# Optimization experiments

Hardware: AMD Instinct MI355X
Metric: run time of the kernel (lower is better)

The kernel has to match this reference:

```python
import jax, jax.numpy as jnp
import numpy as np

B, D, Q, K, C = 1024, 512, 131072, 32, 10
TEMP = 0.1
EPS = 1e-12  # F.normalize eps


def setup_inputs() -> dict:
    key = jax.random.key(0)
    k1, k2, k3 = jax.random.split(key, 3)
    x = jax.random.normal(k1, (B, D), dtype=jnp.float32)
    memory = jax.random.normal(k2, (Q, D), dtype=jnp.float32)
    # queue entries are stored L2-normalized (see update_queue)
    memory = memory / jnp.linalg.norm(memory, axis=1, keepdims=True)
    memory_label = jax.random.randint(k3, (Q,), 0, C, dtype=jnp.int32)
    return {"x": x, "memory": memory, "memory_label": memory_label}


def reference(x, memory, memory_label):
    # cosine similarity: normalize queries, bank already normalized
    xn = x / jnp.maximum(jnp.linalg.norm(x, axis=1, keepdims=True), EPS)
    dist = xn @ memory.T                      # [B, Q]
    sim_weight, sim_indices = jax.lax.top_k(dist, K)   # [B, K]
    sim_labels = memory_label[sim_indices]              # [B, K] gather
    w = jax.nn.softmax(sim_weight / TEMP, axis=1)       # [B, K]
    one_hot = jax.nn.one_hot(sim_labels, C, dtype=w.dtype)  # [B, K, C]
    pred_scores = jnp.einsum('bkc,bk->bc', one_hot, w)       # softmax vote
    return jnp.minimum(pred_scores + 1e-5, 1.0)
```

## Files before the change

### kernel.cpp

```cpp
#include <hip/hip_runtime.h>

typedef unsigned short u16;
typedef unsigned char u8;
typedef __attribute__((ext_vector_type(4))) float f32x4;

#define B_ROWS 1024
#define DIM 512
#define QN 131072
#define TOPK 32
#define NCLS 10
#define TAUS 35.84f
#define CAP 1024
#define FP8SCALE 16.0f

#define S_VMCNT(N) asm volatile("s_waitcnt vmcnt(" #N ")" ::: "memory")
#define S_BAR() asm volatile("s_barrier" ::: "memory")
#define S_LGKM0() asm volatile("s_waitcnt lgkmcnt(0)" ::: "memory")

__device__ __forceinline__ void gload_lds16(const void* gsrc, void* ldst) {
  __builtin_amdgcn_global_load_lds(
      (const __attribute__((address_space(1))) void*)gsrc,
      (__attribute__((address_space(3))) void*)ldst, 16, 0, 0);
}

__device__ __forceinline__ int pk4(float a, float b, float c, float d) {
  int w = __builtin_amdgcn_cvt_pk_fp8_f32(a, b, 0, false);
  w = __builtin_amdgcn_cvt_pk_fp8_f32(c, d, w, true);
  return w;
}

__global__ __launch_bounds__(256) void normalize_x(const float* __restrict__ x,
                                                   float* __restrict__ xn,
                                                   u8* __restrict__ xnb8,
                                                   int* __restrict__ cnt) {
  int row = blockIdx.x;
  int tid = threadIdx.x;
  __shared__ float xs[DIM];
  __shared__ float wsum[4];
  if (tid == 0) cnt[row] = 0;
  float2 v = ((const float2*)(x + (size_t)row * DIM))[tid];
  float ss = v.x * v.x + v.y * v.y;
  #pragma unroll
  for (int o = 32; o; o >>= 1) ss += __shfl_xor(ss, o);
  if ((tid & 63) == 0) wsum[tid >> 6] = ss;
  __syncthreads();
  float tot = wsum[0] + wsum[1] + wsum[2] + wsum[3];
  float scale = 1.0f / fmaxf(sqrtf(tot), 1e-12f);
  float2 o2; o2.x = v.x * scale; o2.y = v.y * scale;
  ((float2*)(xn + (size_t)row * DIM))[tid] = o2;
  xs[2 * tid] = o2.x; xs[2 * tid + 1] = o2.y;
  __syncthreads();
  if (tid < 32) {
    int c = tid >> 2, t4 = tid & 3;
    int k0 = c * 64 + t4 * 8;
    int4 w;
    w.x = pk4(xs[k0+0]*FP8SCALE, xs[k0+1]*FP8SCALE, xs[k0+2]*FP8SCALE, xs[k0+3]*FP8SCALE);
    w.y = pk4(xs[k0+4]*FP8SCALE, xs[k0+5]*FP8SCALE, xs[k0+6]*FP8SCALE, xs[k0+7]*FP8SCALE);
    w.z = pk4(xs[k0+32]*FP8SCALE, xs[k0+33]*FP8SCALE, xs[k0+34]*FP8SCALE, xs[k0+35]*FP8SCALE);
    w.w = pk4(xs[k0+36]*FP8SCALE, xs[k0+37]*FP8SCALE, xs[k0+38]*FP8SCALE, xs[k0+39]*FP8SCALE);
    ((int4*)(xnb8 + (size_t)row * DIM))[tid] = w;
  }
}

__global__ __launch_bounds__(256, 3) void gemm_filter(const u8* __restrict__ xnb8,
                                                      const float* __restrict__ mem,
                                                      int* __restrict__ cnt,
                                                      int* __restrict__ ccol) {
  __shared__ __attribute__((aligned(16))) u8 As[2][16384];
  __shared__ __attribute__((aligned(16))) u8 Bs[2][4096];
  int bid = blockIdx.x;
  int xcd = bid & 7;
  int i = bid >> 3;
  int colt = xcd * 256 + (i >> 2);
  int rowt = i & 3;
  int row0 = rowt * 256;
  int col0 = colt * 64;
  int tid = threadIdx.x;
  int lane = tid & 63;
  int wv = tid >> 6;

  int sg = (tid & 3) ^ ((tid >> 3) & 3);
  const u8* gA[4];
  #pragma unroll
  for (int jj = 0; jj < 4; ++jj) {
    int r = jj * 64 + (tid >> 2);
    gA[jj] = xnb8 + (size_t)(row0 + r) * DIM + sg * 16;
  }
  const float* gB = mem + (size_t)(col0 + (tid >> 2)) * DIM + sg * 8;

  int L = lane & 15;
  int g = lane >> 4;
  int phys = g ^ ((L >> 1) & 3);
  int offA = (wv * 64 + L) * 64 + phys * 16;
  int offB = L * 64 + phys * 16;

  f32x4 acc[4][4];
  #pragma unroll
  for (int m = 0; m < 4; ++m)
    #pragma unroll
    for (int n = 0; n < 4; ++n) acc[m][n] = (f32x4){0.f, 0.f, 0.f, 0.f};

  float4 pb[4];

  auto stageA = [&](int h) {
    int slot = h & 1;
    #pragma unroll
    for (int jj = 0; jj < 4; ++jj)
      gload_lds16(gA[jj] + h * 64, &As[slot][jj * 4096 + tid * 16]);
  };
  auto issuePB = [&](int h) {
    const float4* s = (const float4*)(gB + h * 64);
    pb[0] = s[0]; pb[1] = s[1];
    pb[2] = s[8]; pb[3] = s[9];
  };
  auto writeB = [&](int h) {
    int slot = h & 1;
    int4 w;
    w.x = pk4(pb[0].x*FP8SCALE, pb[0].y*FP8SCALE, pb[0].z*FP8SCALE, pb[0].w*FP8SCALE);
    w.y = pk4(pb[1].x*FP8SCALE, pb[1].y*FP8SCALE, pb[1].z*FP8SCALE, pb[1].w*FP8SCALE);
    w.z = pk4(pb[2].x*FP8SCALE, pb[2].y*FP8SCALE, pb[2].z*FP8SCALE, pb[2].w*FP8SCALE);
    w.w = pk4(pb[3].x*FP8SCALE, pb[3].y*FP8SCALE, pb[3].z*FP8SCALE, pb[3].w*FP8SCALE);
    *(int4*)&Bs[slot][tid * 16] = w;
  };

  union I4L { int4 v; long l[2]; };

  stageA(0); issuePB(0);
  S_VMCNT(0);
  writeB(0);
  issuePB(1);
  S_LGKM0();

  #pragma unroll
  for (int h = 0; h < 8; ++h) {
    if (h < 7) { S_VMCNT(4); }
    else { S_VMCNT(0); }
    S_BAR();
    if (h < 7) stageA(h + 1);
    const u8* Ab = &As[h & 1][0];
    const u8* Bb = &Bs[h & 1][0];
    I4L av[4], bv[4];
    #pragma unroll
    for (int m = 0; m < 4; ++m) av[m].v = *(const int4*)(Ab + offA + m * 1024);
    #pragma unroll
    for (int n = 0; n < 4; ++n) bv[n].v = *(const int4*)(Bb + offB + n * 1024);
    __builtin_amdgcn_s_setprio(1);
    #pragma unroll
    for (int m = 0; m < 4; ++m)
      #pragma unroll
      for (int n = 0; n < 4; ++n)
        acc[m][n] = __builtin_amdgcn_mfma_f32_16x16x32_fp8_fp8(
            av[m].l[0], bv[n].l[0], acc[m][n], 0, 0, 0);
    #pragma unroll
    for (int m = 0; m < 4; ++m)
      #pragma unroll
      for (int n = 0; n < 4; ++n)
        acc[m][n] = __builtin_amdgcn_mfma_f32_16x16x32_fp8_fp8(
            av[m].l[1], bv[n].l[1], acc[m][n], 0, 0, 0);
    __builtin_amdgcn_s_setprio(0);
    if (h < 7) {
      S_VMCNT(4);
      writeB(h + 1);
      if (h < 6) issuePB(h + 2);
      S_LGKM0();
    }
  }

  int rbase = row0 + wv * 64 + (lane >> 4) * 4;
  int cbase = col0 + (lane & 15);
  #pragma unroll
  for (int m = 0; m < 4; ++m)
    #pragma unroll
    for (int n = 0; n < 4; ++n)
      #pragma unroll
      for (int q = 0; q < 4; ++q) {
        float v = acc[m][n][q];
        if (v > TAUS) {
          int grow = rbase + m * 16 + q;
          int gcol = cbase + n * 16;
          int idx = atomicAdd(&cnt[grow], 1);
          if (idx < CAP) ccol[(size_t)grow * CAP + idx] = gcol;
        }
      }
}

__global__ __launch_bounds__(256) void rescore_vote(const float* __restrict__ xn,
                                                    const float* __restrict__ mem,
                                                    const int* __restrict__ labels,
                                                    const int* __restrict__ cnt,
                                                    const int* __restrict__ ccol,
                                                    float* __restrict__ out) {
  int row = blockIdx.x;
  int tid = threadIdx.x;
  int gid = tid >> 4;
  int gl = tid & 15;
  __shared__ __attribute__((aligned(16))) float xs[DIM];
  __shared__ double sv[CAP];
  __shared__ int sc[CAP];
  __shared__ double selv[TOPK];
  __shared__ int selc[TOPK];
  __shared__ double wv32[TOPK];
  __shared__ int slab[TOPK];

  ((float2*)xs)[tid] = ((const float2*)(xn + (size_t)row * DIM))[tid];
  if (tid < TOPK) { selv[tid] = -1e300; selc[tid] = 0; }
  int count = cnt[row];
  if (count > CAP) count = CAP;
  __syncthreads();

  for (int c = gid; c < count; c += 16) {
    int col = ccol[(size_t)row * CAP + c];
    const float4* mp = (const float4*)(mem + (size_t)col * DIM);
    const float4* xp = (const float4*)xs;
    double p = 0.0;
    #pragma unroll
    for (int u = 0; u < 8; ++u) {
      float4 mv = mp[u * 16 + gl];
      float4 xv = xp[u * 16 + gl];
      p += (double)mv.x * xv.x + (double)mv.y * xv.y +
           (double)mv.z * xv.z + (double)mv.w * xv.w;
    }
    #pragma unroll
    for (int o = 8; o; o >>= 1) p += __shfl_xor(p, o);
    if (gl == 0) { sv[c] = p; sc[c] = col; }
  }
  __syncthreads();

  for (int c = tid; c < count; c += 256) {
    double v = sv[c]; int cc = sc[c];
    int r = 0;
    for (int j = 0; j < count; ++j) {
      double vj = sv[j]; int cj = sc[j];
      r += (vj > v) || (vj == v && cj < cc);
    }
    if (r < TOPK) { selv[r] = v; selc[r] = cc; }
  }
  __syncthreads();

  if (tid < TOPK) {
    slab[tid] = labels[selc[tid]];
    double e = exp((selv[tid] - selv[0]) * 10.0);
    double s = e;
    #pragma unroll
    for (int o = 16; o; o >>= 1) s += __shfl_xor(s, o, 32);
    wv32[tid] = e / s;
  }
  __syncthreads();
  if (tid < NCLS) {
    double a = 0.0;
    #pragma unroll
    for (int k = 0; k < TOPK; ++k)
      if (slab[k] == tid) a += wv32[k];
    float r2 = (float)(a + 1e-5);
    out[(size_t)row * NCLS + tid] = fminf(r2, 1.0f);
  }
}

extern "C" void kernel_launch(void* const* d_in, const int* in_sizes, int n_in,
                              void* d_out, int out_size, void* d_ws, size_t ws_size,
                              hipStream_t stream) {
  const float* x = (const float*)d_in[0];
  const float* mem = (const float*)d_in[1];
  const int* labels = (const int*)d_in[2];
  float* out = (float*)d_out;
  char* ws = (char*)d_ws;

  float* xn = (float*)ws;
  u8* xnb8 = (u8*)(ws + 2097152);
  int* cnt = (int*)(ws + 2621440);
  int* ccol = (int*)(ws + 2625536);

  normalize_x<<<dim3(B_ROWS), dim3(256), 0, stream>>>(x, xn, xnb8, cnt);
  gemm_filter<<<dim3((B_ROWS / 256) * (QN / 64)), dim3(256), 0, stream>>>(
      xnb8, mem, cnt, ccol);
  rescore_vote<<<dim3(B_ROWS), dim3(256), 0, stream>>>(xn, mem, labels, cnt,
                                                       ccol, out);
}
```

Baseline: 195.8 us.

## Load A fragments directly from global; stage full B tile in LDS once

The A operand (fp8 normalized queries) is now read straight from global memory into registers with a two-slot software prefetch, replacing the LDS staging path. The full 64x512 B tile is converted to fp8 and written to LDS in one prologue, followed by a single barrier, which removes the per-step barriers and waitcnt choreography. Each wave now issues its own global loads for A, with no sharing through LDS, and the B conversion can no longer overlap the MFMA loop. LDS use drops from 40KB to 32KB per block.

```diff
diff --git a/kernel.cpp b/kernel.cpp
--- a/kernel.cpp
+++ b/kernel.cpp
@@ -12,16 +12,6 @@
 #define TAUS 35.84f
 #define CAP 1024
 #define FP8SCALE 16.0f
-
-#define S_VMCNT(N) asm volatile("s_waitcnt vmcnt(" #N ")" ::: "memory")
-#define S_BAR() asm volatile("s_barrier" ::: "memory")
-#define S_LGKM0() asm volatile("s_waitcnt lgkmcnt(0)" ::: "memory")
-
-__device__ __forceinline__ void gload_lds16(const void* gsrc, void* ldst) {
-  __builtin_amdgcn_global_load_lds(
-      (const __attribute__((address_space(1))) void*)gsrc,
-      (__attribute__((address_space(3))) void*)ldst, 16, 0, 0);
-}
 
 __device__ __forceinline__ int pk4(float a, float b, float c, float d) {
   int w = __builtin_amdgcn_cvt_pk_fp8_f32(a, b, 0, false);
@@ -66,8 +56,7 @@
                                                       const float* __restrict__ mem,
                                                       int* __restrict__ cnt,
                                                       int* __restrict__ ccol) {
-  __shared__ __attribute__((aligned(16))) u8 As[2][16384];
-  __shared__ __attribute__((aligned(16))) u8 Bs[2][4096];
+  __shared__ __attribute__((aligned(16))) u8 Bs[8][4096];
   int bid = blockIdx.x;
   int xcd = bid & 7;
   int i = bid >> 3;
@@ -79,20 +68,34 @@
   int lane = tid & 63;
   int wv = tid >> 6;
 
-  int sg = (tid & 3) ^ ((tid >> 3) & 3);
-  const u8* gA[4];
-  #pragma unroll
-  for (int jj = 0; jj < 4; ++jj) {
-    int r = jj * 64 + (tid >> 2);
-    gA[jj] = xnb8 + (size_t)(row0 + r) * DIM + sg * 16;
-  }
-  const float* gB = mem + (size_t)(col0 + (tid >> 2)) * DIM + sg * 8;
+  {
+    int r = tid >> 2, s = tid & 3;
+    int phys = s ^ ((r >> 1) & 3);
+    const float* src = mem + (size_t)(col0 + r) * DIM + s * 8;
+    u8* dst = &Bs[0][r * 64 + phys * 16];
+    #pragma unroll
+    for (int h = 0; h < 8; ++h) {
+      const float4* sp = (const float4*)(src + h * 64);
+      float4 f0 = sp[0], f1 = sp[1];
+      const float4* sp2 = (const float4*)(src + h * 64 + 32);
+      float4 f2 = sp2[0], f3 = sp2[1];
+      int4 w;
+      w.x = pk4(f0.x*FP8SCALE, f0.y*FP8SCALE, f0.z*FP8SCALE, f0.w*FP8SCALE);
+      w.y = pk4(f1.x*FP8SCALE, f1.y*FP8SCALE, f1.z*FP8SCALE, f1.w*FP8SCALE);
+      w.z = pk4(f2.x*FP8SCALE, f2.y*FP8SCALE, f2.z*FP8SCALE, f2.w*FP8SCALE);
+      w.w = pk4(f3.x*FP8SCALE, f3.y*FP8SCALE, f3.z*FP8SCALE, f3.w*FP8SCALE);
+      *(int4*)(dst + h * 4096) = w;
+    }
+  }
+  __syncthreads();
 
   int L = lane & 15;
   int g = lane >> 4;
-  int phys = g ^ ((L >> 1) & 3);
-  int offA = (wv * 64 + L) * 64 + phys * 16;
-  int offB = L * 64 + phys * 16;
+  const u8* pA[4];
+  #pragma unroll
+  for (int m = 0; m < 4; ++m)
+    pA[m] = xnb8 + (size_t)(row0 + wv * 64 + m * 16 + L) * DIM + g * 16;
+  const u8* pB = &Bs[0][L * 64 + (g ^ ((L >> 1) & 3)) * 16];
 
   f32x4 acc[4][4];
   #pragma unroll
@@ -100,70 +103,37 @@
     #pragma unroll
     for (int n = 0; n < 4; ++n) acc[m][n] = (f32x4){0.f, 0.f, 0.f, 0.f};
 
-  float4 pb[4];
-
-  auto stageA = [&](int h) {
-    int slot = h & 1;
-    #pragma unroll
-    for (int jj = 0; jj < 4; ++jj)
-      gload_lds16(gA[jj] + h * 64, &As[slot][jj * 4096 + tid * 16]);
-  };
-  auto issuePB = [&](int h) {
-    const float4* s = (const float4*)(gB + h * 64);
-    pb[0] = s[0]; pb[1] = s[1];
-    pb[2] = s[8]; pb[3] = s[9];
-  };
-  auto writeB = [&](int h) {
-    int slot = h & 1;
-    int4 w;
-    w.x = pk4(pb[0].x*FP8SCALE, pb[0].y*FP8SCALE, pb[0].z*FP8SCALE, pb[0].w*FP8SCALE);
-    w.y = pk4(pb[1].x*FP8SCALE, pb[1].y*FP8SCALE, pb[1].z*FP8SCALE, pb[1].w*FP8SCALE);
-    w.z = pk4(pb[2].x*FP8SCALE, pb[2].y*FP8SCALE, pb[2].z*FP8SCALE, pb[2].w*FP8SCALE);
-    w.w = pk4(pb[3].x*FP8SCALE, pb[3].y*FP8SCALE, pb[3].z*FP8SCALE, pb[3].w*FP8SCALE);
-    *(int4*)&Bs[slot][tid * 16] = w;
-  };
-
   union I4L { int4 v; long l[2]; };
-
-  stageA(0); issuePB(0);
-  S_VMCNT(0);
-  writeB(0);
-  issuePB(1);
-  S_LGKM0();
+  I4L au0[4], au1[4];
+
+  #pragma unroll
+  for (int m = 0; m < 4; ++m) au0[m].v = *(const int4*)(pA[m] + 0 * 64);
 
   #pragma unroll
   for (int h = 0; h < 8; ++h) {
-    if (h < 7) { S_VMCNT(4); }
-    else { S_VMCNT(0); }
-    S_BAR();
-    if (h < 7) stageA(h + 1);
-    const u8* Ab = &As[h & 1][0];
-    const u8* Bb = &Bs[h & 1][0];
-    I4L av[4], bv[4];
-    #pragma unroll
-    for (int m = 0; m < 4; ++m) av[m].v = *(const int4*)(Ab + offA + m * 1024);
-    #pragma unroll
-    for (int n = 0; n < 4; ++n) bv[n].v = *(const int4*)(Bb + offB + n * 1024);
+    I4L* cur = (h & 1) ? au1 : au0;
+    I4L* nxt = (h & 1) ? au0 : au1;
+    if (h < 7) {
+      #pragma unroll
+      for (int m = 0; m < 4; ++m) nxt[m].v = *(const int4*)(pA[m] + (h + 1) * 64);
+    }
+    I4L bv[4];
+    #pragma unroll
+    for (int n = 0; n < 4; ++n) bv[n].v = *(const int4*)(pB + h * 4096 + n * 1024);
     __builtin_amdgcn_s_setprio(1);
     #pragma unroll
     for (int m = 0; m < 4; ++m)
       #pragma unroll
       for (int n = 0; n < 4; ++n)
         acc[m][n] = __builtin_amdgcn_mfma_f32_16x16x32_fp8_fp8(
-            av[m].l[0], bv[n].l[0], acc[m][n], 0, 0, 0);
+            cur[m].l[0], bv[n].l[0], acc[m][n], 0, 0, 0);
     #pragma unroll
     for (int m = 0; m < 4; ++m)
       #pragma unroll
       for (int n = 0; n < 4; ++n)
         acc[m][n] = __builtin_amdgcn_mfma_f32_16x16x32_fp8_fp8(
-            av[m].l[1], bv[n].l[1], acc[m][n], 0, 0, 0);
+            cur[m].l[1], bv[n].l[1], acc[m][n], 0, 0, 0);
     __builtin_amdgcn_s_setprio(0);
-    if (h < 7) {
-      S_VMCNT(4);
-      writeB(h + 1);
-      if (h < 6) issuePB(h + 2);
-      S_LGKM0();
-    }
   }
 
   int rbase = row0 + wv * 64 + (lane >> 4) * 4;
```

After: 225.1 us. 1.15x slower.
